# Performance work log

Measured on AMD Instinct MI355X. Metric: run time of the kernel, lower is better.

The kernel has to match this reference:

```python
import jax, jax.numpy as jnp
import numpy as np

N_NODES = 50000
N_EDGES = 800000
D_IN = 128
D_OUT = 128


def setup_inputs() -> dict:
    key = jax.random.key(0)
    k1, k2, k3, k4, k5 = jax.random.split(key, 5)
    x = jax.random.normal(k1, (N_NODES, D_IN), dtype=jnp.float32)
    # fc weight, torch Linear convention: [out_dim, in_dim]
    W = jax.random.normal(k2, (D_OUT, D_IN), dtype=jnp.float32) * (1.0 / np.sqrt(D_IN))
    # attn_fc weight: [1, 2*out_dim], no bias
    a = jax.random.normal(k3, (1, 2 * D_OUT), dtype=jnp.float32) * (1.0 / np.sqrt(2 * D_OUT))
    src = jax.random.randint(k4, (N_EDGES,), 0, N_NODES)
    dst = jax.random.randint(k5, (N_EDGES,), 0, N_NODES)
    return {"x": x, "W": W, "a": a, "src": src, "dst": dst}


def reference(x, W, a, src, dst):
    # h = fc(x)
    h = x @ W.T  # [N, D_OUT]
    # attn_fc(cat([h_src, h_dst])) == h_src @ a[:D] + h_dst @ a[D:] (linear, no bias),
    # so precompute per-node scalars instead of materializing [E, 2*D_OUT].
    a_src = a[0, :D_OUT]
    a_dst = a[0, D_OUT:]
    s = h @ a_src  # [N]
    d = h @ a_dst  # [N]
    e = jax.nn.sigmoid(s[src] + d[dst])[:, None]  # [E, 1]
    msg = e * h[src]  # [E, D_OUT]  edge gather + weight
    # reduce: f[v] = sum over incoming edges of e * h_src
    f = jax.ops.segment_sum(msg, dst, num_segments=N_NODES)  # [N, D_OUT]
    return f
```

## Files before the change

kernel.cpp:

```cpp
#include <hip/hip_runtime.h>
#include <hip/hip_bf16.h>
#include <stdint.h>

#define NN 50000
#define NE 800000
#define DD 128
#define NBKT 782
#define BCH 4096
#define BGRID ((NE + BCH - 1) / BCH)
#define CAP 1280
#define SPILL_CAP 32768
#define GROWS 64
#define GGRID ((NN + GROWS - 1) / GROWS)

typedef __attribute__((ext_vector_type(8))) unsigned short ushort8;
typedef __attribute__((ext_vector_type(8))) short short8;
typedef __attribute__((ext_vector_type(4))) float f32x4;

__device__ inline uint32_t cvtpk(float lo, float hi) {
    uint32_t r;
    asm("v_cvt_pk_bf16_f32 %0, %1, %2" : "=v"(r) : "v"(lo), "v"(hi));
    return r;
}
__device__ inline float bf_lo(uint32_t u) { return __uint_as_float(u << 16); }
__device__ inline float bf_hi(uint32_t u) { return __uint_as_float(u & 0xffff0000u); }

__global__ __launch_bounds__(256) void prep_k(const float* __restrict__ W,
                                              uint16_t* __restrict__ Wb,
                                              int* __restrict__ cntg) {
    int t = threadIdx.x;
    if (blockIdx.x == 0) {
        for (int k = t; k < NBKT + 4; k += 256) cntg[k] = 0;
    }
    int i = blockIdx.x * 256 + t;
    if (i < DD * DD) {
        uint32_t u = __float_as_uint(W[i]);
        Wb[i] = (uint16_t)((u + 0x7fffu + ((u >> 16) & 1u)) >> 16);
    }
}

__global__ __launch_bounds__(256) void fused_k(const float* __restrict__ x,
                                               const uint16_t* __restrict__ Wb,
                                               const float* __restrict__ a,
                                               const int* __restrict__ src,
                                               const int* __restrict__ dst,
                                               uint16_t* __restrict__ hb,
                                               float* __restrict__ sArr,
                                               float* __restrict__ dArr,
                                               int* __restrict__ cntg,
                                               int* __restrict__ scnt,
                                               uint32_t* __restrict__ rec,
                                               uint2* __restrict__ spill) {
    __shared__ int lh[NBKT];
    __shared__ int gb[NBKT];
    const int t = threadIdx.x;

    if ((int)blockIdx.x < GGRID) {
        const int l = t & 63, wid = t >> 6;
        const int r0 = blockIdx.x * GROWS;
        const int lr = l & 15, lk = l >> 4;

        f32x4 acc[8];
        #pragma unroll
        for (int c = 0; c < 8; ++c) acc[c] = f32x4{0.f, 0.f, 0.f, 0.f};

        const int arow = r0 + wid * 16 + lr;
        const int lrow = (arow < NN) ? arow : (NN - 1);
        const float* xp = x + (size_t)lrow * DD + lk * 8;

        #pragma unroll
        for (int kc = 0; kc < 4; ++kc) {
            float4 v0 = *(const float4*)(xp + kc * 32);
            float4 v1 = *(const float4*)(xp + kc * 32 + 4);
            union { uint32_t u[4]; short8 s; } A;
            A.u[0] = cvtpk(v0.x, v0.y); A.u[1] = cvtpk(v0.z, v0.w);
            A.u[2] = cvtpk(v1.x, v1.y); A.u[3] = cvtpk(v1.z, v1.w);
            #pragma unroll
            for (int c = 0; c < 8; ++c) {
                int col = c * 16 + lr;
                short8 bf_ = *(const short8*)(Wb + (size_t)col * DD + kc * 32 + lk * 8);
                acc[c] = __builtin_amdgcn_mfma_f32_16x16x32_bf16(A.s, bf_, acc[c], 0, 0, 0);
            }
        }

        float avs[8], avd[8];
        #pragma unroll
        for (int c = 0; c < 8; ++c) {
            avs[c] = a[c * 16 + lr];
            avd[c] = a[DD + c * 16 + lr];
        }
        #pragma unroll
        for (int i = 0; i < 4; ++i) {
            float ps = 0.f, pd = 0.f;
            #pragma unroll
            for (int c = 0; c < 8; ++c) {
                ps = fmaf(acc[c][i], avs[c], ps);
                pd = fmaf(acc[c][i], avd[c], pd);
            }
            #pragma unroll
            for (int o = 8; o > 0; o >>= 1) {
                ps += __shfl_xor(ps, o);
                pd += __shfl_xor(pd, o);
            }
            int row = r0 + wid * 16 + lk * 4 + i;
            if (lr == 0 && row < NN) { sArr[row] = ps; dArr[row] = pd; }
        }

        #pragma unroll
        for (int i = 0; i < 4; ++i) {
            int row = r0 + wid * 16 + lk * 4 + i;
            if (row < NN) {
                union { uint32_t u[4]; ushort8 s; } H;
                H.u[0] = cvtpk(acc[0][i], acc[1][i]);
                H.u[1] = cvtpk(acc[2][i], acc[3][i]);
                H.u[2] = cvtpk(acc[4][i], acc[5][i]);
                H.u[3] = cvtpk(acc[6][i], acc[7][i]);
                *(ushort8*)(hb + (size_t)row * DD + lr * 8) = H.s;
            }
        }
    } else {
        int bb = blockIdx.x - GGRID;
        for (int k = t; k < NBKT; k += 256) lh[k] = 0;
        __syncthreads();
        int base = bb * BCH;
        unsigned pk[16]; int bk[16];
        #pragma unroll
        for (int i = 0; i < 16; ++i) {
            int idx = base + i * 256 + t;
            if (idx < NE) {
                int s_ = src[idx], d_ = dst[idx];
                bk[i] = d_ >> 6;
                pk[i] = ((unsigned)(d_ & 63) << 16) | (unsigned)s_;
                atomicAdd(&lh[bk[i]], 1);
            } else bk[i] = -1;
        }
        __syncthreads();
        for (int k = t; k < NBKT; k += 256) {
            int c = lh[k];
            lh[k] = 0;
            if (c) gb[k] = atomicAdd(&cntg[k], c);
        }
        __syncthreads();
        #pragma unroll
        for (int i = 0; i < 16; ++i) {
            if (bk[i] >= 0) {
                int sl = atomicAdd(&lh[bk[i]], 1);
                int p = gb[bk[i]] + sl;
                if (p < CAP) {
                    rec[(size_t)bk[i] * CAP + p] = pk[i];
                } else {
                    int sp = atomicAdd(scnt, 1);
                    if (sp < SPILL_CAP)
                        spill[sp] = make_uint2(pk[i] & 0xffffu,
                                               (unsigned)(bk[i] * 64 + (int)(pk[i] >> 16)));
                }
            }
        }
    }
}

__global__ __launch_bounds__(512) void bsort_agg_k(const uint16_t* __restrict__ hb,
                                                   const float* __restrict__ sA,
                                                   const float* __restrict__ dA,
                                                   const int* __restrict__ cntg,
                                                   const uint32_t* __restrict__ rec,
                                                   const int* __restrict__ scnt,
                                                   const uint2* __restrict__ spill,
                                                   float* __restrict__ out) {
    __shared__ uint32_t srt[CAP];
    __shared__ float    eL[CAP];
    __shared__ float dAl[64];
    __shared__ int h64[64];
    __shared__ int s65[65];
    __shared__ int curw[64];
    int t = threadIdx.x, l = t & 63, wid = t >> 6;
    int b = blockIdx.x;
    int cnt = cntg[b]; if (cnt > CAP) cnt = CAP;
    int beg = b * CAP;
    int n0 = b * 64;
    int ns = *scnt; if (ns > SPILL_CAP) ns = SPILL_CAP;
    if (t < 64) {
        h64[t] = 0;
        int n = n0 + t;
        dAl[t] = (n < NN) ? dA[n] : 0.f;
    }
    __syncthreads();

    uint32_t rc[3]; float er[3]; int nrc = 0;
    for (int j = t; j < cnt; j += 512) {
        uint32_t r = rec[beg + j];
        rc[nrc] = r;
        atomicAdd(&h64[r >> 16], 1);
        float z = sA[r & 0xffffu] + dAl[r >> 16];
        er[nrc] = 1.f / (1.f + __expf(-z));
        ++nrc;
    }
    __syncthreads();
    if (wid == 0) {
        int v = h64[l];
        int inc = v;
        #pragma unroll
        for (int o = 1; o < 64; o <<= 1) {
            int nb = __shfl_up(inc, o);
            if (l >= o) inc += nb;
        }
        s65[l + 1] = inc;
        if (l == 0) s65[0] = 0;
        curw[l] = inc - v;
    }
    __syncthreads();
    for (int k = 0; k < nrc; ++k) {
        uint32_t r = rc[k];
        int p = atomicAdd(&curw[r >> 16], 1);
        srt[p] = r;
        eL[p] = er[k];
    }
    __syncthreads();

    const int q = l >> 4, sl = l & 15;
    const char* hbp = (const char*)hb;
    #pragma unroll 1
    for (int rr = 0; rr < 8; ++rr) {
        int d = wid * 8 + rr;
        int n = n0 + d;
        if (n >= NN) break;
        int js = s65[d], je = s65[d + 1];
        float acc[8] = {0.f,0.f,0.f,0.f,0.f,0.f,0.f,0.f};
        for (int j = js; j < je; j += 8) {
            int j0 = j + q, j1 = j + 4 + q;
            bool v0 = j0 < je, v1 = j1 < je;
            uint32_t r0 = srt[v0 ? j0 : js];
            uint32_t r1 = srt[v1 ? j1 : js];
            float e0 = v0 ? eL[j0] : 0.f;
            float e1 = v1 ? eL[j1] : 0.f;
            uint4 u0 = *(const uint4*)(hbp + (size_t)(r0 & 0xffffu) * 256 + sl * 16);
            uint4 u1 = *(const uint4*)(hbp + (size_t)(r1 & 0xffffu) * 256 + sl * 16);
            acc[0] = fmaf(e0, bf_lo(u0.x), acc[0]); acc[1] = fmaf(e0, bf_hi(u0.x), acc[1]);
            acc[2] = fmaf(e0, bf_lo(u0.y), acc[2]); acc[3] = fmaf(e0, bf_hi(u0.y), acc[3]);
            acc[4] = fmaf(e0, bf_lo(u0.z), acc[4]); acc[5] = fmaf(e0, bf_hi(u0.z), acc[5]);
            acc[6] = fmaf(e0, bf_lo(u0.w), acc[6]); acc[7] = fmaf(e0, bf_hi(u0.w), acc[7]);
            acc[0] = fmaf(e1, bf_lo(u1.x), acc[0]); acc[1] = fmaf(e1, bf_hi(u1.x), acc[1]);
            acc[2] = fmaf(e1, bf_lo(u1.y), acc[2]); acc[3] = fmaf(e1, bf_hi(u1.y), acc[3]);
            acc[4] = fmaf(e1, bf_lo(u1.z), acc[4]); acc[5] = fmaf(e1, bf_hi(u1.z), acc[5]);
            acc[6] = fmaf(e1, bf_lo(u1.w), acc[6]); acc[7] = fmaf(e1, bf_hi(u1.w), acc[7]);
        }
        #pragma unroll
        for (int k = 0; k < 8; ++k) {
            acc[k] += __shfl_xor(acc[k], 16);
            acc[k] += __shfl_xor(acc[k], 32);
        }
        if (ns > 0) {
            for (int i = 0; i < ns; ++i) {
                uint2 sp = spill[i];
                if ((int)sp.y == n) {
                    float z = sA[sp.x] + dAl[d];
                    float e = 1.f / (1.f + __expf(-z));
                    uint4 u = *(const uint4*)(hbp + (size_t)sp.x * 256 + sl * 16);
                    acc[0] = fmaf(e, bf_lo(u.x), acc[0]); acc[1] = fmaf(e, bf_hi(u.x), acc[1]);
                    acc[2] = fmaf(e, bf_lo(u.y), acc[2]); acc[3] = fmaf(e, bf_hi(u.y), acc[3]);
                    acc[4] = fmaf(e, bf_lo(u.z), acc[4]); acc[5] = fmaf(e, bf_hi(u.z), acc[5]);
                    acc[6] = fmaf(e, bf_lo(u.w), acc[6]); acc[7] = fmaf(e, bf_hi(u.w), acc[7]);
                }
            }
        }
        float* orow = out + (size_t)n * DD;
        orow[(2 * q) * 16 + sl]     = acc[2 * q];
        orow[(2 * q + 1) * 16 + sl] = acc[2 * q + 1];
    }
}

__global__ __launch_bounds__(256) void edge_atomic_k(const int* __restrict__ src, const int* __restrict__ dst,
                                                     const float* __restrict__ sArr, const float* __restrict__ dArr,
                                                     const uint32_t* __restrict__ hb, float* __restrict__ out) {
    int wid = threadIdx.x >> 6, l = threadIdx.x & 63;
    int e = blockIdx.x * 4 + wid;
    if (e >= NE) return;
    int sv = src[e], dv = dst[e];
    float z = sArr[sv] + dArr[dv];
    float ev = 1.0f / (1.0f + __expf(-z));
    uint32_t u = hb[(size_t)sv * 64 + l];
    int colx = 32 * (l & 3) + (l >> 2);
    atomicAdd(&out[(size_t)dv * DD + colx],      ev * bf_lo(u));
    atomicAdd(&out[(size_t)dv * DD + colx + 16], ev * bf_hi(u));
}

extern "C" void kernel_launch(void* const* d_in, const int* in_sizes, int n_in,
                              void* d_out, int out_size, void* d_ws, size_t ws_size,
                              hipStream_t stream) {
    const float* x  = (const float*)d_in[0];
    const float* W  = (const float*)d_in[1];
    const float* a  = (const float*)d_in[2];
    const int* src  = (const int*)d_in[3];
    const int* dst  = (const int*)d_in[4];
    float* out = (float*)d_out;

    char* p = (char*)d_ws;
    uint16_t* hb = (uint16_t*)p;            p += (size_t)NN * DD * 2;
    uint16_t* Wb = (uint16_t*)p;            p += (size_t)DD * DD * 2;
    float* sA    = (float*)p;               p += (size_t)NN * 4;
    float* dA    = (float*)p;               p += (size_t)NN * 4;
    int*   cntg  = (int*)p;                 p += (size_t)NBKT * 4;
    int*   scnt  = (int*)p;                 p += 16;
    uint32_t* rec = (uint32_t*)(((uintptr_t)p + 15) & ~(uintptr_t)15);
    p = (char*)(rec + (size_t)NBKT * CAP);
    uint2* spill = (uint2*)p;               p += (size_t)SPILL_CAP * 8;
    size_t need  = (size_t)(p - (char*)d_ws);

    if (ws_size >= need) {
        prep_k<<<64, 256, 0, stream>>>(W, Wb, cntg);
        fused_k<<<GGRID + BGRID, 256, 0, stream>>>(x, Wb, a, src, dst,
                                                   hb, sA, dA, cntg, scnt, rec, spill);
        bsort_agg_k<<<NBKT, 512, 0, stream>>>(hb, sA, dA, cntg, rec, scnt, spill, out);
    } else {
        hipMemsetAsync(out, 0, sizeof(float) * (size_t)NN * DD, stream);
        prep_k<<<64, 256, 0, stream>>>(W, Wb, cntg);
        fused_k<<<GGRID, 256, 0, stream>>>(x, Wb, a, src, dst,
                                           hb, sA, dA, cntg, scnt, rec, spill);
        edge_atomic_k<<<NE / 4, 256, 0, stream>>>(src, dst, sA, dA, (const uint32_t*)hb, out);
    }
}
```

Before: 72.98 us.

## Phase edge aggregation by source-index range for L2 locality of gathers

Edges in each destination block are now sorted by a (source-range phase, destination) bin instead of by destination only. The aggregation loop walks the eight phases in order, keeping 64 accumulators per lane live for all eight rows. The aim is for concurrently running blocks to gather h rows from the same source range and so reuse L2/MALL. The cost is much higher register pressure (64 float accumulators per lane), which may reduce occupancy, plus more scan work and finer-grained bins with poorer lane utilization.

```diff
diff --git a/kernel.cpp b/kernel.cpp
--- a/kernel.cpp
+++ b/kernel.cpp
@@ -12,6 +12,7 @@
 #define SPILL_CAP 32768
 #define GROWS 64
 #define GGRID ((NN + GROWS - 1) / GROWS)
+#define NPH 8
 
 typedef __attribute__((ext_vector_type(8))) unsigned short ushort8;
 typedef __attribute__((ext_vector_type(8))) short short8;
@@ -170,84 +171,107 @@
     __shared__ uint32_t srt[CAP];
     __shared__ float    eL[CAP];
     __shared__ float dAl[64];
-    __shared__ int h64[64];
-    __shared__ int s65[65];
-    __shared__ int curw[64];
+    __shared__ int hbin[NPH * 64];
+    __shared__ int soff[NPH * 64 + 1];
+    __shared__ int curw[NPH * 64];
     int t = threadIdx.x, l = t & 63, wid = t >> 6;
     int b = blockIdx.x;
     int cnt = cntg[b]; if (cnt > CAP) cnt = CAP;
     int beg = b * CAP;
     int n0 = b * 64;
     int ns = *scnt; if (ns > SPILL_CAP) ns = SPILL_CAP;
+    for (int k = t; k < NPH * 64; k += 512) hbin[k] = 0;
     if (t < 64) {
-        h64[t] = 0;
         int n = n0 + t;
         dAl[t] = (n < NN) ? dA[n] : 0.f;
     }
     __syncthreads();
 
-    uint32_t rc[3]; float er[3]; int nrc = 0;
+    uint32_t rc[3]; float er[3]; int bn[3]; int nrc = 0;
     for (int j = t; j < cnt; j += 512) {
         uint32_t r = rec[beg + j];
-        rc[nrc] = r;
-        atomicAdd(&h64[r >> 16], 1);
-        float z = sA[r & 0xffffu] + dAl[r >> 16];
+        int d = (int)(r >> 16);
+        int bin = (((r >> 13) & (NPH - 1)) << 6) | d;
+        rc[nrc] = r; bn[nrc] = bin;
+        atomicAdd(&hbin[bin], 1);
+        float z = sA[r & 0xffffu] + dAl[d];
         er[nrc] = 1.f / (1.f + __expf(-z));
         ++nrc;
     }
     __syncthreads();
     if (wid == 0) {
-        int v = h64[l];
-        int inc = v;
+        int base8 = l * 8;
+        int v[8]; int s = 0;
+        #pragma unroll
+        for (int k = 0; k < 8; ++k) { v[k] = hbin[base8 + k]; s += v[k]; }
+        int inc = s;
         #pragma unroll
         for (int o = 1; o < 64; o <<= 1) {
             int nb = __shfl_up(inc, o);
             if (l >= o) inc += nb;
         }
-        s65[l + 1] = inc;
-        if (l == 0) s65[0] = 0;
-        curw[l] = inc - v;
+        int run = inc - s;
+        #pragma unroll
+        for (int k = 0; k < 8; ++k) { soff[base8 + k] = run; curw[base8 + k] = run; run += v[k]; }
+        if (l == 63) soff[NPH * 64] = run;
     }
     __syncthreads();
     for (int k = 0; k < nrc; ++k) {
-        uint32_t r = rc[k];
-        int p = atomicAdd(&curw[r >> 16], 1);
-        srt[p] = r;
+        int p = atomicAdd(&curw[bn[k]], 1);
+        srt[p] = rc[k];
         eL[p] = er[k];
     }
     __syncthreads();
 
     const int q = l >> 4, sl = l & 15;
     const char* hbp = (const char*)hb;
+    float acc[8][8];
+    #pragma unroll
+    for (int rr = 0; rr < 8; ++rr)
+        #pragma unroll
+        for (int k = 0; k < 8; ++k) acc[rr][k] = 0.f;
+
     #pragma unroll 1
+    for (int ph = 0; ph < NPH; ++ph) {
+        #pragma unroll
+        for (int rr = 0; rr < 8; ++rr) {
+            int d = wid * 8 + rr;
+            int bin = (ph << 6) | d;
+            int js = soff[bin], je = soff[bin + 1];
+            for (int j = js; j < je; j += 8) {
+                int j0 = j + q;
+                if (j0 < je) {
+                    uint32_t r0 = srt[j0];
+                    float e0 = eL[j0];
+                    uint4 u0 = *(const uint4*)(hbp + (size_t)(r0 & 0xffffu) * 256 + sl * 16);
+                    acc[rr][0] = fmaf(e0, bf_lo(u0.x), acc[rr][0]); acc[rr][1] = fmaf(e0, bf_hi(u0.x), acc[rr][1]);
+                    acc[rr][2] = fmaf(e0, bf_lo(u0.y), acc[rr][2]); acc[rr][3] = fmaf(e0, bf_hi(u0.y), acc[rr][3]);
+                    acc[rr][4] = fmaf(e0, bf_lo(u0.z), acc[rr][4]); acc[rr][5] = fmaf(e0, bf_hi(u0.z), acc[rr][5]);
+                    acc[rr][6] = fmaf(e0, bf_lo(u0.w), acc[rr][6]); acc[rr][7] = fmaf(e0, bf_hi(u0.w), acc[rr][7]);
+                }
+                int j1 = j + 4 + q;
+                if (j1 < je) {
+                    uint32_t r1 = srt[j1];
+                    float e1 = eL[j1];
+                    uint4 u1 = *(const uint4*)(hbp + (size_t)(r1 & 0xffffu) * 256 + sl * 16);
+                    acc[rr][0] = fmaf(e1, bf_lo(u1.x), acc[rr][0]); acc[rr][1] = fmaf(e1, bf_hi(u1.x), acc[rr][1]);
+                    acc[rr][2] = fmaf(e1, bf_lo(u1.y), acc[rr][2]); acc[rr][3] = fmaf(e1, bf_hi(u1.y), acc[rr][3]);
+                    acc[rr][4] = fmaf(e1, bf_lo(u1.z), acc[rr][4]); acc[rr][5] = fmaf(e1, bf_hi(u1.z), acc[rr][5]);
+                    acc[rr][6] = fmaf(e1, bf_lo(u1.w), acc[rr][6]); acc[rr][7] = fmaf(e1, bf_hi(u1.w), acc[rr][7]);
+                }
+            }
+        }
+    }
+
+    #pragma unroll
     for (int rr = 0; rr < 8; ++rr) {
         int d = wid * 8 + rr;
         int n = n0 + d;
-        if (n >= NN) break;
-        int js = s65[d], je = s65[d + 1];
-        float acc[8] = {0.f,0.f,0.f,0.f,0.f,0.f,0.f,0.f};
-        for (int j = js; j < je; j += 8) {
-            int j0 = j + q, j1 = j + 4 + q;
-            bool v0 = j0 < je, v1 = j1 < je;
-            uint32_t r0 = srt[v0 ? j0 : js];
-            uint32_t r1 = srt[v1 ? j1 : js];
-            float e0 = v0 ? eL[j0] : 0.f;
-            float e1 = v1 ? eL[j1] : 0.f;
-            uint4 u0 = *(const uint4*)(hbp + (size_t)(r0 & 0xffffu) * 256 + sl * 16);
-            uint4 u1 = *(const uint4*)(hbp + (size_t)(r1 & 0xffffu) * 256 + sl * 16);
-            acc[0] = fmaf(e0, bf_lo(u0.x), acc[0]); acc[1] = fmaf(e0, bf_hi(u0.x), acc[1]);
-            acc[2] = fmaf(e0, bf_lo(u0.y), acc[2]); acc[3] = fmaf(e0, bf_hi(u0.y), acc[3]);
-            acc[4] = fmaf(e0, bf_lo(u0.z), acc[4]); acc[5] = fmaf(e0, bf_hi(u0.z), acc[5]);
-            acc[6] = fmaf(e0, bf_lo(u0.w), acc[6]); acc[7] = fmaf(e0, bf_hi(u0.w), acc[7]);
-            acc[0] = fmaf(e1, bf_lo(u1.x), acc[0]); acc[1] = fmaf(e1, bf_hi(u1.x), acc[1]);
-            acc[2] = fmaf(e1, bf_lo(u1.y), acc[2]); acc[3] = fmaf(e1, bf_hi(u1.y), acc[3]);
-            acc[4] = fmaf(e1, bf_lo(u1.z), acc[4]); acc[5] = fmaf(e1, bf_hi(u1.z), acc[5]);
-            acc[6] = fmaf(e1, bf_lo(u1.w), acc[6]); acc[7] = fmaf(e1, bf_hi(u1.w), acc[7]);
-        }
+        if (n >= NN) continue;
         #pragma unroll
         for (int k = 0; k < 8; ++k) {
-            acc[k] += __shfl_xor(acc[k], 16);
-            acc[k] += __shfl_xor(acc[k], 32);
+            acc[rr][k] += __shfl_xor(acc[rr][k], 16);
+            acc[rr][k] += __shfl_xor(acc[rr][k], 32);
         }
         if (ns > 0) {
             for (int i = 0; i < ns; ++i) {
@@ -256,16 +280,18 @@
                     float z = sA[sp.x] + dAl[d];
                     float e = 1.f / (1.f + __expf(-z));
                     uint4 u = *(const uint4*)(hbp + (size_t)sp.x * 256 + sl * 16);
-                    acc[0] = fmaf(e, bf_lo(u.x), acc[0]); acc[1] = fmaf(e, bf_hi(u.x), acc[1]);
-                    acc[2] = fmaf(e, bf_lo(u.y), acc[2]); acc[3] = fmaf(e, bf_hi(u.y), acc[3]);
-                    acc[4] = fmaf(e, bf_lo(u.z), acc[4]); acc[5] = fmaf(e, bf_hi(u.z), acc[5]);
-                    acc[6] = fmaf(e, bf_lo(u.w), acc[6]); acc[7] = fmaf(e, bf_hi(u.w), acc[7]);
+                    acc[rr][0] = fmaf(e, bf_lo(u.x), acc[rr][0]); acc[rr][1] = fmaf(e, bf_hi(u.x), acc[rr][1]);
+                    acc[rr][2] = fmaf(e, bf_lo(u.y), acc[rr][2]); acc[rr][3] = fmaf(e, bf_hi(u.y), acc[rr][3]);
+                    acc[rr][4] = fmaf(e, bf_lo(u.z), acc[rr][4]); acc[rr][5] = fmaf(e, bf_hi(u.z), acc[rr][5]);
+                    acc[rr][6] = fmaf(e, bf_lo(u.w), acc[rr][6]); acc[rr][7] = fmaf(e, bf_hi(u.w), acc[rr][7]);
                 }
             }
         }
+        float vx = (q == 0) ? acc[rr][0] : (q == 1) ? acc[rr][2] : (q == 2) ? acc[rr][4] : acc[rr][6];
+        float vy = (q == 0) ? acc[rr][1] : (q == 1) ? acc[rr][3] : (q == 2) ? acc[rr][5] : acc[rr][7];
         float* orow = out + (size_t)n * DD;
-        orow[(2 * q) * 16 + sl]     = acc[2 * q];
-        orow[(2 * q + 1) * 16 + sl] = acc[2 * q + 1];
+        orow[(2 * q) * 16 + sl]     = vx;
+        orow[(2 * q + 1) * 16 + sl] = vy;
     }
 }
 
```

New measurement: 110.2 us. +51.0%, slower.
